# Optimization experiments

Hardware: AMD Instinct MI355X
Metric: run time of the kernel (lower is better)

## Reference

```python
import jax, jax.numpy as jnp
import numpy as np

FACTOR = 2  # self.factor
KSIZE = 3   # causal_fusion depthwise conv kernel size


def causal_fusion(x, w, b):
    # x: [BH, C, N]; depthwise causal conv over the node axis (left pad k-1)
    k = w.shape[-1]
    out = jax.lax.conv_general_dilated(
        x, w, window_strides=(1,), padding=[(k - 1, 0)],
        dimension_numbers=('NCH', 'OIH', 'NCH'),
        feature_group_count=x.shape[1])
    return out + b[None, :, None]


def setup_inputs() -> dict:
    key = jax.random.key(0)
    ks = jax.random.split(key, 4)
    B, N, L, H, E = 4, 64, 128, 8, 32
    queries = jax.random.normal(ks[0], (B, N, L, H, E), jnp.float32)
    keys = jax.random.normal(ks[1], (B, N, L, H, E), jnp.float32)
    values = jax.random.normal(ks[2], (B, N, L, H, E), jnp.float32)
    attn_mask = jnp.zeros((1,), jnp.bool_)
    C = E * L  # 4096 channels seen by causal_fusion
    w_cf = jax.random.normal(ks[3], (C, 1, KSIZE), jnp.float32) * 0.05
    b_cf = jnp.zeros((C,), jnp.float32)
    return {"queries": queries, "keys": keys, "values": values,
            "attn_mask": attn_mask, "w_cf": w_cf, "b_cf": b_cf}


def reference(queries, keys, values, attn_mask, w_cf, b_cf):
    B, N, L, H, E = queries.shape  # S == L, so no pad/slice branch taken

    # --- FFT cross-correlation: corr[b,n,h,e,:] = irfft(rfft(mean_n q) * conj(rfft(k)))
    qm = jnp.broadcast_to(jnp.mean(queries, axis=1, keepdims=True), queries.shape)
    qp = jnp.transpose(qm, (0, 1, 3, 4, 2))      # [B,N,H,E,L]
    kp = jnp.transpose(keys, (0, 1, 3, 4, 2))    # [B,N,H,E,L]
    vp = jnp.transpose(values, (0, 1, 3, 4, 2))  # [B,N,H,E,L]
    corr = jnp.fft.irfft(jnp.fft.rfft(qp, axis=-1) * jnp.conj(jnp.fft.rfft(kp, axis=-1)), n=L, axis=-1)

    # --- align_speed: top-k delays over channel-mean corr, circular roll of values
    mean_corr = jnp.mean(corr, axis=3)                      # [B,N,H,L]
    weight, delay_idx = jax.lax.top_k(mean_corr, FACTOR)    # [B,N,H,F]
    delay = L - delay_idx                                   # values in [1, L]
    ar = jnp.arange(L)
    aligned = []
    for i in range(FACTOR):
        idx = (ar[None, None, None, None, :] + delay[..., i][..., None, None]) % L  # [B,N,H,1,L]
        idx = jnp.broadcast_to(idx, vp.shape)
        aligned.append(jnp.take_along_axis(vp, idx, axis=-1))  # [B,N,H,E,L]

    BH = B * H
    delay_bh = jnp.transpose(delay, (0, 2, 1, 3)).reshape(BH, N, FACTOR)
    weight_bh = jnp.transpose(weight, (0, 2, 1, 3)).reshape(BH, N, FACTOR)

    # --- per-factor: sort nodes by delay -> causal fusion over nodes -> unsort
    causal_agg = []
    for i in range(FACTOR):
        indices = jnp.argsort(delay_bh[..., i], axis=-1)               # [BH,N]
        av = jnp.transpose(aligned[i], (0, 2, 1, 3, 4)).reshape(BH, N, E, L)
        av = av * jax.nn.sigmoid(weight_bh[..., i])[:, :, None, None]
        sorted_av = jnp.take_along_axis(av, indices[:, :, None, None], axis=1)
        x = jnp.transpose(sorted_av.reshape(BH, N, E * L), (0, 2, 1))  # [BH,E*L,N]
        x = causal_fusion(x, w_cf, b_cf)
        x = jnp.transpose(x, (0, 2, 1)).reshape(BH, N, E, L)
        rev = jnp.argsort(indices, axis=-1)
        x = jnp.take_along_axis(x, rev[:, :, None, None], axis=1)
        causal_agg.append(jnp.transpose(x.reshape(B, H, N, E, L), (0, 2, 1, 3, 4)))  # [B,N,H,E,L]

    # --- align_back_speed: inverse circular shift, mean over factors
    delay_back = L - delay  # [B,N,H,F]
    agg = jnp.zeros_like(causal_agg[0])
    for i in range(FACTOR):
        idx = (ar[None, None, None, None, :] + delay_back[..., i][..., None, None]) % L
        idx = jnp.broadcast_to(idx, causal_agg[i].shape)
        agg = agg + jnp.take_along_axis(causal_agg[i], idx, axis=-1)
    agg = agg / FACTOR

    V = jnp.transpose(agg, (0, 1, 4, 2, 3))  # [B,N,L,H,E]
    return V
```

## Files before the change

### kernel.cpp

```cpp
#include <hip/hip_runtime.h>
#include <math.h>

#define B_ 4
#define N_ 64
#define L_ 128
#define H_ 8
#define E_ 32
#define SC_ 8

typedef __attribute__((ext_vector_type(8))) short short8;
typedef __attribute__((ext_vector_type(4))) float f32x4;

__device__ __forceinline__ unsigned short f2bf(float x) {
    union { float f; unsigned u; } c; c.f = x;
    unsigned r = (c.u + 0x7fffu + ((c.u >> 16) & 1u)) >> 16;
    return (unsigned short)r;
}
__device__ __forceinline__ float bf2f(unsigned short h) {
    union { unsigned u; float f; } c; c.u = ((unsigned)h) << 16;
    return c.f;
}

__global__ __launch_bounds__(256) void k_qmean(const float* __restrict__ q,
                                               float* __restrict__ qm,
                                               const float* __restrict__ w,
                                               const float* __restrict__ bias,
                                               float* __restrict__ wT,
                                               float* __restrict__ bT,
                                               int* __restrict__ wcnt) {
    int blk = blockIdx.x;
    int b = blk >> 7, t = blk & 127;
    int tid = threadIdx.x;
    int c4 = tid & 63;
    int nq = tid >> 6;
    __shared__ double red[4][256];
    const f32x4* p = (const f32x4*)(q + (((size_t)(b * N_)) * L_ + t) * 256);
    double s0 = 0, s1 = 0, s2 = 0, s3 = 0;
    #pragma unroll 4
    for (int n = nq * 16; n < nq * 16 + 16; ++n) {
        f32x4 v = p[(size_t)n * 8192 + c4];
        s0 += (double)v.x; s1 += (double)v.y; s2 += (double)v.z; s3 += (double)v.w;
    }
    red[nq][c4 * 4 + 0] = s0;
    red[nq][c4 * 4 + 1] = s1;
    red[nq][c4 * 4 + 2] = s2;
    red[nq][c4 * 4 + 3] = s3;
    __syncthreads();
    int c = tid;
    double s = red[0][c] + red[1][c] + red[2][c] + red[3][c];
    qm[((size_t)b * 256 + c) * L_ + t] = (float)(s * (1.0 / 64.0));

    if (blk < 16) {
        int k = blk * 256 + tid;
        int e = k & 31, lp = k >> 5;
        int cc = e * L_ + lp;
        wT[k]        = w[cc * 3 + 0];
        wT[4096 + k] = w[cc * 3 + 1];
        wT[8192 + k] = w[cc * 3 + 2];
        bT[k]        = bias[cc];
    }
    if (blk == 16 && tid == 0) *wcnt = 0;
}

__global__ __launch_bounds__(512) void k_corr(const float* __restrict__ keys,
                                              const float* __restrict__ qm,
                                              float* __restrict__ part) {
    int blk = blockIdx.x;
    int sc = blk & 7; int bh = blk >> 3; int h = bh & 7; int b = bh >> 3;
    __shared__ unsigned short Ahi[4][64][40];
    __shared__ unsigned short Alo[4][64][40];
    __shared__ unsigned short Qhi[128][40];
    __shared__ unsigned short Qlo[128][40];
    int tid = threadIdx.x;
    int lane = tid & 63, w = tid >> 6;
    int mg = w & 1, ng = w >> 1;

    {
        int e = tid >> 4; int tq = (tid & 15) * 4;
        const float* qp = qm + ((size_t)b * 256 + h * 32 + e) * 128;
        #pragma unroll
        for (int hf = 0; hf < 2; ++hf) {
            int t0 = tq + hf * 64;
            float4 v = *(const float4*)(qp + t0);
            float vv[4] = {v.x, v.y, v.z, v.w};
            #pragma unroll
            for (int j = 0; j < 4; ++j) {
                unsigned short hi = f2bf(vv[j]);
                Qhi[t0 + j][e] = hi;
                Qlo[t0 + j][e] = f2bf(vv[j] - bf2f(hi));
            }
        }
    }
    int sn = tid >> 3; int se = (tid & 7) * 4;
    const float* kbase = keys + ((size_t)(b * N_ + sn) * L_) * 256 + h * 32 + se;
    #pragma unroll
    for (int p = 0; p < 2; ++p) {
        float4 v = *(const float4*)(kbase + (size_t)(sc * 16 + p) * 256);
        float vv[4] = {v.x, v.y, v.z, v.w};
        ushort4 h4, l4;
        unsigned short* hp = (unsigned short*)&h4;
        unsigned short* lp = (unsigned short*)&l4;
        #pragma unroll
        for (int j = 0; j < 4; ++j) {
            hp[j] = f2bf(vv[j]);
            lp[j] = f2bf(vv[j] - bf2f(hp[j]));
        }
        *(ushort4*)&Ahi[p][sn][se] = h4;
        *(ushort4*)&Alo[p][sn][se] = l4;
    }
    __syncthreads();

    f32x4 acc[2][2];
    #pragma unroll
    for (int i = 0; i < 2; ++i)
        #pragma unroll
        for (int j = 0; j < 2; ++j)
            acc[i][j] = (f32x4){0.f, 0.f, 0.f, 0.f};

    int eb = (lane >> 4) * 8;
    int rA0 = (mg * 2) * 16 + (lane & 15);
    int rA1 = rA0 + 16;
    int tau0 = (ng * 2) * 16 + (lane & 15);
    int tau1 = tau0 + 16;

    for (int it = 0; it < 8; ++it) {
        float4 stg0, stg1;
        if (it < 7) {
            stg0 = *(const float4*)(kbase + (size_t)(sc * 16 + 2 * it + 2) * 256);
            stg1 = *(const float4*)(kbase + (size_t)(sc * 16 + 2 * it + 3) * 256);
        }
        #pragma unroll
        for (int sp = 0; sp < 2; ++sp) {
            int p = 2 * it + sp;
            int slot = p & 3;
            int s = sc * 16 + p;
            short8 ah0 = *(const short8*)&Ahi[slot][rA0][eb];
            short8 ah1 = *(const short8*)&Ahi[slot][rA1][eb];
            short8 al0 = *(const short8*)&Alo[slot][rA0][eb];
            short8 al1 = *(const short8*)&Alo[slot][rA1][eb];
            int t0 = (s + tau0) & 127;
            int t1 = (s + tau1) & 127;
            short8 bh0 = *(const short8*)&Qhi[t0][eb];
            short8 bh1 = *(const short8*)&Qhi[t1][eb];
            short8 bl0 = *(const short8*)&Qlo[t0][eb];
            short8 bl1 = *(const short8*)&Qlo[t1][eb];
            acc[0][0] = __builtin_amdgcn_mfma_f32_16x16x32_bf16(ah0, bh0, acc[0][0], 0, 0, 0);
            acc[0][1] = __builtin_amdgcn_mfma_f32_16x16x32_bf16(ah0, bh1, acc[0][1], 0, 0, 0);
            acc[1][0] = __builtin_amdgcn_mfma_f32_16x16x32_bf16(ah1, bh0, acc[1][0], 0, 0, 0);
            acc[1][1] = __builtin_amdgcn_mfma_f32_16x16x32_bf16(ah1, bh1, acc[1][1], 0, 0, 0);
            acc[0][0] = __builtin_amdgcn_mfma_f32_16x16x32_bf16(ah0, bl0, acc[0][0], 0, 0, 0);
            acc[0][1] = __builtin_amdgcn_mfma_f32_16x16x32_bf16(ah0, bl1, acc[0][1], 0, 0, 0);
            acc[1][0] = __builtin_amdgcn_mfma_f32_16x16x32_bf16(ah1, bl0, acc[1][0], 0, 0, 0);
            acc[1][1] = __builtin_amdgcn_mfma_f32_16x16x32_bf16(ah1, bl1, acc[1][1], 0, 0, 0);
            acc[0][0] = __builtin_amdgcn_mfma_f32_16x16x32_bf16(al0, bh0, acc[0][0], 0, 0, 0);
            acc[0][1] = __builtin_amdgcn_mfma_f32_16x16x32_bf16(al0, bh1, acc[0][1], 0, 0, 0);
            acc[1][0] = __builtin_amdgcn_mfma_f32_16x16x32_bf16(al1, bh0, acc[1][0], 0, 0, 0);
            acc[1][1] = __builtin_amdgcn_mfma_f32_16x16x32_bf16(al1, bh1, acc[1][1], 0, 0, 0);
        }
        if (it < 7) {
            #pragma unroll
            for (int sp = 0; sp < 2; ++sp) {
                int p = 2 * it + 2 + sp;
                int slot = p & 3;
                float4 v = sp ? stg1 : stg0;
                float vv[4] = {v.x, v.y, v.z, v.w};
                ushort4 h4, l4;
                unsigned short* hp = (unsigned short*)&h4;
                unsigned short* lp = (unsigned short*)&l4;
                #pragma unroll
                for (int j = 0; j < 4; ++j) {
                    hp[j] = f2bf(vv[j]);
                    lp[j] = f2bf(vv[j] - bf2f(hp[j]));
                }
                *(ushort4*)&Ahi[slot][sn][se] = h4;
                *(ushort4*)&Alo[slot][sn][se] = l4;
            }
        }
        __syncthreads();
    }

    #pragma unroll
    for (int i = 0; i < 2; ++i) {
        int mt = mg * 2 + i;
        #pragma unroll
        for (int j = 0; j < 2; ++j) {
            int nt = ng * 2 + j;
            int tau = nt * 16 + (lane & 15);
            #pragma unroll
            for (int r = 0; r < 4; ++r) {
                int n = mt * 16 + (lane >> 4) * 4 + r;
                part[((((size_t)sc * B_ + b) * N_ + n) * H_ + h) * L_ + tau] = acc[i][j][r];
            }
        }
    }
}

__global__ __launch_bounds__(64) void k_topk(const float* __restrict__ part,
                                             int* __restrict__ didx,
                                             float* __restrict__ sig,
                                             int* __restrict__ flags,
                                             int* __restrict__ wlist,
                                             int* __restrict__ wcnt) {
    int blk = blockIdx.x;
    int lane = threadIdx.x;
    size_t rb = (size_t)blk * L_;
    const size_t stride = (size_t)B_ * N_ * H_ * L_;
    double s0 = 0.0, s1 = 0.0;
    for (int sc = 0; sc < SC_; ++sc) {
        s0 += (double)part[sc * stride + rb + lane];
        s1 += (double)part[sc * stride + rb + lane + 64];
    }
    float v0 = (float)(s0 * (1.0 / 32.0));
    float v1 = (float)(s1 * (1.0 / 32.0));

    float bv = v0; int bi = lane;
    if (v1 > v0) { bv = v1; bi = lane + 64; }
    #pragma unroll
    for (int m = 32; m; m >>= 1) {
        float ov = __shfl_xor(bv, m, 64);
        int   oi = __shfl_xor(bi, m, 64);
        if (ov > bv || (ov == bv && oi < bi)) { bv = ov; bi = oi; }
    }
    int i1 = bi; float w1v = bv;

    float c0 = (lane == i1) ? -INFINITY : v0;
    float c1 = (lane + 64 == i1) ? -INFINITY : v1;
    float bv2 = c0; int bi2 = lane;
    if (c1 > c0) { bv2 = c1; bi2 = lane + 64; }
    #pragma unroll
    for (int m = 32; m; m >>= 1) {
        float ov = __shfl_xor(bv2, m, 64);
        int   oi = __shfl_xor(bi2, m, 64);
        if (ov > bv2 || (ov == bv2 && oi < bi2)) { bv2 = ov; bi2 = oi; }
    }
    int i2 = bi2; float w2v = bv2;

    float d0 = (lane == i1 || lane == i2) ? -INFINITY : v0;
    float d1 = (lane + 64 == i1 || lane + 64 == i2) ? -INFINITY : v1;
    float bv3 = fmaxf(d0, d1);
    #pragma unroll
    for (int m = 32; m; m >>= 1) bv3 = fmaxf(bv3, __shfl_xor(bv3, m, 64));

    if (lane == 0) {
        didx[blk * 2 + 0] = i1;
        didx[blk * 2 + 1] = i2;
        sig[blk * 2 + 0] = 1.f / (1.f + expf(-w1v));
        sig[blk * 2 + 1] = 1.f / (1.f + expf(-w2v));
        int fl = (w2v - bv3 < 1e-3f) ? 1 : 0;
        flags[blk] = fl;
        if (fl) { int s = atomicAdd(wcnt, 1); wlist[s] = blk; }
    }
}

__global__ __launch_bounds__(256) void k_fixup(const float* __restrict__ keys,
                                               const float* __restrict__ qm,
                                               const int* __restrict__ wlist,
                                               const int* __restrict__ wcnt,
                                               double* __restrict__ vvg) {
    int cnt = *wcnt;
    __shared__ float ks_t[L_][E_];
    __shared__ float qs_t[L_][E_];
    __shared__ double red[16][17];
    int tid = threadIdx.x;
    for (int wi = blockIdx.x; wi < cnt * 8; wi += gridDim.x) {
        int row = wlist[wi >> 3]; int tg = wi & 7;
        int h = row & 7; int r = row >> 3; int n = r & 63; int b = r >> 6;
        __syncthreads();
        for (int idx = tid; idx < 1024; idx += 256) {
            int s = idx >> 3, e4 = idx & 7;
            *(float4*)&ks_t[s][e4 * 4] =
                *(const float4*)&keys[(((size_t)(b * N_ + n)) * L_ + s) * 256 + h * E_ + e4 * 4];
            int e = idx >> 5, t4 = (idx & 31) * 4;
            float4 v = *(const float4*)&qm[((size_t)b * 256 + h * E_ + e) * L_ + t4];
            float vvj[4] = {v.x, v.y, v.z, v.w};
            #pragma unroll
            for (int j = 0; j < 4; ++j) {
                int t = t4 + j;
                int col = ((((e >> 2) ^ (t & 7)) << 2) | (e & 3));
                qs_t[t][col] = vvj[j];
            }
        }
        __syncthreads();
        int tau = tg * 16 + (tid & 15);
        int g = tid >> 4;
        double a0 = 0, a1 = 0, a2 = 0, a3 = 0, a4 = 0, a5 = 0, a6 = 0, a7 = 0;
        #pragma unroll 2
        for (int s = g * 8; s < g * 8 + 8; ++s) {
            int t = (s + tau) & 127;
            int x = t & 7;
            #pragma unroll
            for (int e4 = 0; e4 < 8; e4 += 2) {
                float4 k0 = *(const float4*)&ks_t[s][e4 * 4];
                float4 k1 = *(const float4*)&ks_t[s][e4 * 4 + 4];
                float4 q0 = *(const float4*)&qs_t[t][(e4 ^ x) << 2];
                float4 q1 = *(const float4*)&qs_t[t][((e4 + 1) ^ x) << 2];
                a0 = fma((double)k0.x, (double)q0.x, a0);
                a1 = fma((double)k0.y, (double)q0.y, a1);
                a2 = fma((double)k0.z, (double)q0.z, a2);
                a3 = fma((double)k0.w, (double)q0.w, a3);
                a4 = fma((double)k1.x, (double)q1.x, a4);
                a5 = fma((double)k1.y, (double)q1.y, a5);
                a6 = fma((double)k1.z, (double)q1.z, a6);
                a7 = fma((double)k1.w, (double)q1.w, a7);
            }
        }
        red[g][tid & 15] = ((a0 + a1) + (a2 + a3)) + ((a4 + a5) + (a6 + a7));
        __syncthreads();
        if (tid < 16) {
            double s = 0;
            #pragma unroll
            for (int gg = 0; gg < 16; ++gg) s += red[gg][tid];
            vvg[(size_t)row * L_ + tg * 16 + tid] = s;
        }
    }
}

__global__ __launch_bounds__(128) void k_sort(const int* __restrict__ didx,
                                              const float* __restrict__ sig,
                                              const int* __restrict__ flags,
                                              const double* __restrict__ vvg,
                                              int4* __restrict__ gparam_i,
                                              f32x4* __restrict__ gparam_f) {
    int bh = blockIdx.x;
    int b = bh >> 3, h = bh & 7;
    int tid = threadIdx.x; int i = tid >> 6; int n = tid & 63;
    __shared__ int ds[2][64];
    __shared__ int pm[2][64];
    __shared__ int dival[2][64];
    __shared__ float sigval[2][64];
    {
        int row = (b * 64 + n) * 8 + h;
        int dv = didx[row * 2 + i];
        dival[i][n] = dv;
        sigval[i][n] = sig[row * 2 + i];
        ds[i][n] = 128 - dv;
    }
    __syncthreads();

    if (tid < 64) {
        int lane = tid;
        int myflag = flags[(b * 64 + lane) * 8 + h];
        unsigned long long msk = __ballot(myflag != 0);
        while (msk) {
            int nn = __ffsll((long long)msk) - 1; msk &= msk - 1;
            int row = (b * 64 + nn) * 8 + h;
            float v0 = (float)(vvg[(size_t)row * L_ + lane] * (1.0 / 32.0));
            float v1 = (float)(vvg[(size_t)row * L_ + lane + 64] * (1.0 / 32.0));
            float bv = v0; int bi = lane;
            if (v1 > v0) { bv = v1; bi = lane + 64; }
            #pragma unroll
            for (int m = 32; m; m >>= 1) {
                float ov = __shfl_xor(bv, m, 64);
                int   oi = __shfl_xor(bi, m, 64);
                if (ov > bv || (ov == bv && oi < bi)) { bv = ov; bi = oi; }
            }
            int i1 = bi; float w1v = bv;
            float c0 = (lane == i1) ? -INFINITY : v0;
            float c1 = (lane + 64 == i1) ? -INFINITY : v1;
            float bv2 = c0; int bi2 = lane;
            if (c1 > c0) { bv2 = c1; bi2 = lane + 64; }
            #pragma unroll
            for (int m = 32; m; m >>= 1) {
                float ov = __shfl_xor(bv2, m, 64);
                int   oi = __shfl_xor(bi2, m, 64);
                if (ov > bv2 || (ov == bv2 && oi < bi2)) { bv2 = ov; bi2 = oi; }
            }
            if (lane == 0) {
                dival[0][nn] = i1;      ds[0][nn] = 128 - i1;
                dival[1][nn] = bi2;     ds[1][nn] = 128 - bi2;
                sigval[0][nn] = 1.f / (1.f + expf(-w1v));
                sigval[1][nn] = 1.f / (1.f + expf(-bv2));
            }
        }
    }
    __syncthreads();

    int d = ds[i][n];
    int rank = 0;
    for (int m = 0; m < 64; ++m) {
        int dm = ds[i][m];
        rank += (dm < d || (dm == d && m < n)) ? 1 : 0;
    }
    pm[i][rank] = n;
    __syncthreads();
    int p1v = (rank >= 1) ? pm[i][rank - 1] : -1;
    int p2v = (rank >= 2) ? pm[i][rank - 2] : -1;

    int din = dival[i][n];
    int pq1 = (p1v >= 0) ? p1v : n;
    int pq2 = (p2v >= 0) ? p2v : n;
    int d1 = (p1v >= 0) ? ((din - dival[i][p1v]) & 127) : 0;
    int d2 = (p2v >= 0) ? ((din - dival[i][p2v]) & 127) : 0;
    float s1 = (p1v >= 0) ? sigval[i][p1v] : 0.f;
    float s2 = (p2v >= 0) ? sigval[i][p2v] : 0.f;
    int blko = (b * 64 + n) * 8 + h;
    gparam_i[blko * 2 + i] = make_int4(pq1, pq2, d1, d2);
    gparam_f[blko * 2 + i] = (f32x4){s1, s2, sigval[i][n], (float)din};
}

__global__ __launch_bounds__(256, 3) void k_out(const float* __restrict__ values,
                                                const float* __restrict__ wT,
                                                const float* __restrict__ bT,
                                                const int4* __restrict__ gparam_i,
                                                const f32x4* __restrict__ gparam_f,
                                                float* __restrict__ out) {
    int bid = blockIdx.x;
    int h = bid & 7;
    int q = (bid >> 3) & 3;
    int n = (bid >> 5) & 63;
    int b = bid >> 11;
    int blk = (b * 64 + n) * 8 + h;
    int tid = threadIdx.x; int e4 = tid & 7; int tq = tid >> 3;
    int t = q * 32 + tq;

    int4  gi0 = gparam_i[blk * 2 + 0];
    int4  gi1 = gparam_i[blk * 2 + 1];
    f32x4 gf0 = gparam_f[blk * 2 + 0];
    f32x4 gf1 = gparam_f[blk * 2 + 1];
    int di0 = (int)gf0.w, di1 = (int)gf1.w;

    const f32x4* v4 = (const f32x4*)values;
    const f32x4* w4 = (const f32x4*)wT;
    const f32x4* b4 = (const f32x4*)bT;
    f32x4* o4 = (f32x4*)out;
    const size_t base = ((size_t)b * N_) * L_ * 64 + h * 8 + e4;

    f32x4 vs  = v4[base + ((size_t)n * L_ + t) * 64];
    f32x4 va1 = v4[base + ((size_t)gi0.x * L_ + ((t + gi0.z) & 127)) * 64];
    f32x4 va2 = v4[base + ((size_t)gi0.y * L_ + ((t + gi0.w) & 127)) * 64];
    f32x4 vb1 = v4[base + ((size_t)gi1.x * L_ + ((t + gi1.z) & 127)) * 64];
    f32x4 vb2 = v4[base + ((size_t)gi1.y * L_ + ((t + gi1.w) & 127)) * 64];
    int wo0 = ((t + di0) & 127) * 8 + e4;
    int wo1 = ((t + di1) & 127) * 8 + e4;
    f32x4 bb0 = b4[wo0], w0a = w4[wo0], w1a = w4[1024 + wo0], w2a = w4[2048 + wo0];
    f32x4 bb1 = b4[wo1], w0b = w4[wo1], w1b = w4[1024 + wo1], w2b = w4[2048 + wo1];

    f32x4 acc = bb0 + bb1;
    acc += w2a * (gf0.z * vs);
    acc += w1a * (gf0.x * va1);
    acc += w0a * (gf0.y * va2);
    acc += w2b * (gf1.z * vs);
    acc += w1b * (gf1.x * vb1);
    acc += w0b * (gf1.y * vb2);
    o4[base + ((size_t)n * L_ + t) * 64] = acc * 0.5f;
}

extern "C" void kernel_launch(void* const* d_in, const int* in_sizes, int n_in,
                              void* d_out, int out_size, void* d_ws, size_t ws_size,
                              hipStream_t stream) {
    const float* queries = (const float*)d_in[0];
    const float* keys    = (const float*)d_in[1];
    const float* values  = (const float*)d_in[2];
    const float* w_cf = (const float*)d_in[4];
    const float* b_cf = (const float*)d_in[5];
    float* out = (float*)d_out;

    float* ws    = (float*)d_ws;
    float* qm    = ws;
    float* wT    = qm + 131072;
    float* bT    = wT + 12288;
    float* sigp  = bT + 4096;
    int*   didxp = (int*)(sigp + 4096);
    int*   flags = didxp + 4096;
    int*   wlist = flags + 2048;
    int*   wcnt  = wlist + 2048;
    double* vvg  = (double*)(wcnt + 4);
    int4*  gpi   = (int4*)(vvg + 2048 * 128);
    f32x4* gpf   = (f32x4*)(gpi + 4096);

    float* part = (float*)d_out;

    k_qmean <<<512,  256, 0, stream>>>(queries, qm, w_cf, b_cf, wT, bT, wcnt);
    k_corr  <<<256,  512, 0, stream>>>(keys, qm, part);
    k_topk  <<<2048, 64,  0, stream>>>(part, didxp, sigp, flags, wlist, wcnt);
    k_fixup <<<256,  256, 0, stream>>>(keys, qm, wlist, wcnt, vvg);
    k_sort  <<<32,   128, 0, stream>>>(didxp, sigp, flags, vvg, gpi, gpf);
    k_out   <<<8192, 256, 0, stream>>>(values, wT, bT, gpi, gpf, out);
}
```

Before: 71.97 us.

## Fuse top-k, double-precision fixup and sort into one per-(b,h) select kernel

Replaces the k_topk, k_fixup and k_sort kernels with a single k_select kernel: one 1024-thread block per (batch, head). It reduces the partial correlations, picks the top-2 delays, recomputes ambiguous rows in double precision, and ranks and sorts delays, all in shared memory. This removes two kernel launches, the global atomics and work list, and the global round-trips for flags, indices and fixup sums. The cost is that the stage now runs on only 32 blocks, and flagged rows are recomputed one after another inside a block instead of spread across 256 blocks.

```diff
diff --git a/kernel.cpp b/kernel.cpp
--- a/kernel.cpp
+++ b/kernel.cpp
@@ -26,8 +26,7 @@
                                                const float* __restrict__ w,
                                                const float* __restrict__ bias,
                                                float* __restrict__ wT,
-                                               float* __restrict__ bT,
-                                               int* __restrict__ wcnt) {
+                                               float* __restrict__ bT) {
     int blk = blockIdx.x;
     int b = blk >> 7, t = blk & 127;
     int tid = threadIdx.x;
@@ -59,7 +58,6 @@
         wT[8192 + k] = w[cc * 3 + 2];
         bT[k]        = bias[cc];
     }
-    if (blk == 16 && tid == 0) *wcnt = 0;
 }
 
 __global__ __launch_bounds__(512) void k_corr(const float* __restrict__ keys,
@@ -195,157 +193,122 @@
     }
 }
 
-__global__ __launch_bounds__(64) void k_topk(const float* __restrict__ part,
-                                             int* __restrict__ didx,
-                                             float* __restrict__ sig,
-                                             int* __restrict__ flags,
-                                             int* __restrict__ wlist,
-                                             int* __restrict__ wcnt) {
-    int blk = blockIdx.x;
-    int lane = threadIdx.x;
-    size_t rb = (size_t)blk * L_;
-    const size_t stride = (size_t)B_ * N_ * H_ * L_;
-    double s0 = 0.0, s1 = 0.0;
-    for (int sc = 0; sc < SC_; ++sc) {
-        s0 += (double)part[sc * stride + rb + lane];
-        s1 += (double)part[sc * stride + rb + lane + 64];
-    }
-    float v0 = (float)(s0 * (1.0 / 32.0));
-    float v1 = (float)(s1 * (1.0 / 32.0));
-
-    float bv = v0; int bi = lane;
-    if (v1 > v0) { bv = v1; bi = lane + 64; }
-    #pragma unroll
-    for (int m = 32; m; m >>= 1) {
-        float ov = __shfl_xor(bv, m, 64);
-        int   oi = __shfl_xor(bi, m, 64);
-        if (ov > bv || (ov == bv && oi < bi)) { bv = ov; bi = oi; }
-    }
-    int i1 = bi; float w1v = bv;
-
-    float c0 = (lane == i1) ? -INFINITY : v0;
-    float c1 = (lane + 64 == i1) ? -INFINITY : v1;
-    float bv2 = c0; int bi2 = lane;
-    if (c1 > c0) { bv2 = c1; bi2 = lane + 64; }
-    #pragma unroll
-    for (int m = 32; m; m >>= 1) {
-        float ov = __shfl_xor(bv2, m, 64);
-        int   oi = __shfl_xor(bi2, m, 64);
-        if (ov > bv2 || (ov == bv2 && oi < bi2)) { bv2 = ov; bi2 = oi; }
-    }
-    int i2 = bi2; float w2v = bv2;
-
-    float d0 = (lane == i1 || lane == i2) ? -INFINITY : v0;
-    float d1 = (lane + 64 == i1 || lane + 64 == i2) ? -INFINITY : v1;
-    float bv3 = fmaxf(d0, d1);
-    #pragma unroll
-    for (int m = 32; m; m >>= 1) bv3 = fmaxf(bv3, __shfl_xor(bv3, m, 64));
-
-    if (lane == 0) {
-        didx[blk * 2 + 0] = i1;
-        didx[blk * 2 + 1] = i2;
-        sig[blk * 2 + 0] = 1.f / (1.f + expf(-w1v));
-        sig[blk * 2 + 1] = 1.f / (1.f + expf(-w2v));
-        int fl = (w2v - bv3 < 1e-3f) ? 1 : 0;
-        flags[blk] = fl;
-        if (fl) { int s = atomicAdd(wcnt, 1); wlist[s] = blk; }
-    }
-}
-
-__global__ __launch_bounds__(256) void k_fixup(const float* __restrict__ keys,
-                                               const float* __restrict__ qm,
-                                               const int* __restrict__ wlist,
-                                               const int* __restrict__ wcnt,
-                                               double* __restrict__ vvg) {
-    int cnt = *wcnt;
+__global__ __launch_bounds__(1024) void k_select(const float* __restrict__ part,
+                                                 const float* __restrict__ keys,
+                                                 const float* __restrict__ qm,
+                                                 int4* __restrict__ gparam_i,
+                                                 f32x4* __restrict__ gparam_f) {
+    int bh = blockIdx.x;
+    int b = bh >> 3, h = bh & 7;
+    int tid = threadIdx.x;
+    int lane = tid & 63, w = tid >> 6;
+
     __shared__ float ks_t[L_][E_];
     __shared__ float qs_t[L_][E_];
-    __shared__ double red[16][17];
-    int tid = threadIdx.x;
-    for (int wi = blockIdx.x; wi < cnt * 8; wi += gridDim.x) {
-        int row = wlist[wi >> 3]; int tg = wi & 7;
-        int h = row & 7; int r = row >> 3; int n = r & 63; int b = r >> 6;
+    __shared__ double vv[8][L_];
+    __shared__ int   didxL[2][64];
+    __shared__ float sigL[2][64];
+    __shared__ int   flagL[64];
+    __shared__ int   ds[2][64];
+    __shared__ int   pm[2][64];
+
+    {
+        int e = tid >> 5, t4 = (tid & 31) * 4;
+        float4 v = *(const float4*)&qm[((size_t)b * 256 + h * E_ + e) * L_ + t4];
+        float vvj[4] = {v.x, v.y, v.z, v.w};
+        #pragma unroll
+        for (int j = 0; j < 4; ++j) {
+            int t = t4 + j;
+            int col = ((((e >> 2) ^ (t & 7)) << 2) | (e & 3));
+            qs_t[t][col] = vvj[j];
+        }
+    }
+
+    const size_t stride = (size_t)B_ * N_ * H_ * L_;
+    for (int k = 0; k < 4; ++k) {
+        int n = w * 4 + k;
+        size_t rb = (((size_t)b * 64 + n) * 8 + h) * (size_t)L_;
+        double s0 = 0.0, s1 = 0.0;
+        for (int sc = 0; sc < SC_; ++sc) {
+            s0 += (double)part[sc * stride + rb + lane];
+            s1 += (double)part[sc * stride + rb + lane + 64];
+        }
+        float v0 = (float)(s0 * (1.0 / 32.0));
+        float v1 = (float)(s1 * (1.0 / 32.0));
+
+        float bv = v0; int bi = lane;
+        if (v1 > v0) { bv = v1; bi = lane + 64; }
+        #pragma unroll
+        for (int m = 32; m; m >>= 1) {
+            float ov = __shfl_xor(bv, m, 64);
+            int   oi = __shfl_xor(bi, m, 64);
+            if (ov > bv || (ov == bv && oi < bi)) { bv = ov; bi = oi; }
+        }
+        int i1 = bi; float w1v = bv;
+
+        float c0 = (lane == i1) ? -INFINITY : v0;
+        float c1 = (lane + 64 == i1) ? -INFINITY : v1;
+        float bv2 = c0; int bi2 = lane;
+        if (c1 > c0) { bv2 = c1; bi2 = lane + 64; }
+        #pragma unroll
+        for (int m = 32; m; m >>= 1) {
+            float ov = __shfl_xor(bv2, m, 64);
+            int   oi = __shfl_xor(bi2, m, 64);
+            if (ov > bv2 || (ov == bv2 && oi < bi2)) { bv2 = ov; bi2 = oi; }
+        }
+        int i2 = bi2; float w2v = bv2;
+
+        float d0 = (lane == i1 || lane == i2) ? -INFINITY : v0;
+        float d1 = (lane + 64 == i1 || lane + 64 == i2) ? -INFINITY : v1;
+        float bv3 = fmaxf(d0, d1);
+        #pragma unroll
+        for (int m = 32; m; m >>= 1) bv3 = fmaxf(bv3, __shfl_xor(bv3, m, 64));
+
+        if (lane == 0) {
+            didxL[0][n] = i1; didxL[1][n] = i2;
+            sigL[0][n] = 1.f / (1.f + expf(-w1v));
+            sigL[1][n] = 1.f / (1.f + expf(-w2v));
+            flagL[n] = (w2v - bv3 < 1e-3f) ? 1 : 0;
+        }
+    }
+    __syncthreads();
+
+    for (int nn = 0; nn < 64; ++nn) {
+        if (!flagL[nn]) continue;
+        {
+            int s = tid >> 3, e4 = tid & 7;
+            *(float4*)&ks_t[s][e4 * 4] =
+                *(const float4*)&keys[(((size_t)(b * N_ + nn)) * L_ + s) * 256 + h * E_ + e4 * 4];
+        }
         __syncthreads();
-        for (int idx = tid; idx < 1024; idx += 256) {
-            int s = idx >> 3, e4 = idx & 7;
-            *(float4*)&ks_t[s][e4 * 4] =
-                *(const float4*)&keys[(((size_t)(b * N_ + n)) * L_ + s) * 256 + h * E_ + e4 * 4];
-            int e = idx >> 5, t4 = (idx & 31) * 4;
-            float4 v = *(const float4*)&qm[((size_t)b * 256 + h * E_ + e) * L_ + t4];
-            float vvj[4] = {v.x, v.y, v.z, v.w};
-            #pragma unroll
-            for (int j = 0; j < 4; ++j) {
-                int t = t4 + j;
-                int col = ((((e >> 2) ^ (t & 7)) << 2) | (e & 3));
-                qs_t[t][col] = vvj[j];
-            }
-        }
-        __syncthreads();
-        int tau = tg * 16 + (tid & 15);
-        int g = tid >> 4;
+        int tau = tid & 127, g = tid >> 7;
+        int sh = g >> 2, eo = g & 3;
         double a0 = 0, a1 = 0, a2 = 0, a3 = 0, a4 = 0, a5 = 0, a6 = 0, a7 = 0;
-        #pragma unroll 2
-        for (int s = g * 8; s < g * 8 + 8; ++s) {
+        for (int s = sh * 64; s < sh * 64 + 64; ++s) {
             int t = (s + tau) & 127;
             int x = t & 7;
-            #pragma unroll
-            for (int e4 = 0; e4 < 8; e4 += 2) {
-                float4 k0 = *(const float4*)&ks_t[s][e4 * 4];
-                float4 k1 = *(const float4*)&ks_t[s][e4 * 4 + 4];
-                float4 q0 = *(const float4*)&qs_t[t][(e4 ^ x) << 2];
-                float4 q1 = *(const float4*)&qs_t[t][((e4 + 1) ^ x) << 2];
-                a0 = fma((double)k0.x, (double)q0.x, a0);
-                a1 = fma((double)k0.y, (double)q0.y, a1);
-                a2 = fma((double)k0.z, (double)q0.z, a2);
-                a3 = fma((double)k0.w, (double)q0.w, a3);
-                a4 = fma((double)k1.x, (double)q1.x, a4);
-                a5 = fma((double)k1.y, (double)q1.y, a5);
-                a6 = fma((double)k1.z, (double)q1.z, a6);
-                a7 = fma((double)k1.w, (double)q1.w, a7);
-            }
-        }
-        red[g][tid & 15] = ((a0 + a1) + (a2 + a3)) + ((a4 + a5) + (a6 + a7));
+            float4 k0 = *(const float4*)&ks_t[s][eo * 8];
+            float4 k1 = *(const float4*)&ks_t[s][eo * 8 + 4];
+            float4 q0 = *(const float4*)&qs_t[t][((2 * eo) ^ x) << 2];
+            float4 q1 = *(const float4*)&qs_t[t][((2 * eo + 1) ^ x) << 2];
+            a0 = fma((double)k0.x, (double)q0.x, a0);
+            a1 = fma((double)k0.y, (double)q0.y, a1);
+            a2 = fma((double)k0.z, (double)q0.z, a2);
+            a3 = fma((double)k0.w, (double)q0.w, a3);
+            a4 = fma((double)k1.x, (double)q1.x, a4);
+            a5 = fma((double)k1.y, (double)q1.y, a5);
+            a6 = fma((double)k1.z, (double)q1.z, a6);
+            a7 = fma((double)k1.w, (double)q1.w, a7);
+        }
+        vv[g][tau] = ((a0 + a1) + (a2 + a3)) + ((a4 + a5) + (a6 + a7));
         __syncthreads();
-        if (tid < 16) {
-            double s = 0;
-            #pragma unroll
-            for (int gg = 0; gg < 16; ++gg) s += red[gg][tid];
-            vvg[(size_t)row * L_ + tg * 16 + tid] = s;
-        }
-    }
-}
-
-__global__ __launch_bounds__(128) void k_sort(const int* __restrict__ didx,
-                                              const float* __restrict__ sig,
-                                              const int* __restrict__ flags,
-                                              const double* __restrict__ vvg,
-                                              int4* __restrict__ gparam_i,
-                                              f32x4* __restrict__ gparam_f) {
-    int bh = blockIdx.x;
-    int b = bh >> 3, h = bh & 7;
-    int tid = threadIdx.x; int i = tid >> 6; int n = tid & 63;
-    __shared__ int ds[2][64];
-    __shared__ int pm[2][64];
-    __shared__ int dival[2][64];
-    __shared__ float sigval[2][64];
-    {
-        int row = (b * 64 + n) * 8 + h;
-        int dv = didx[row * 2 + i];
-        dival[i][n] = dv;
-        sigval[i][n] = sig[row * 2 + i];
-        ds[i][n] = 128 - dv;
-    }
-    __syncthreads();
-
-    if (tid < 64) {
-        int lane = tid;
-        int myflag = flags[(b * 64 + lane) * 8 + h];
-        unsigned long long msk = __ballot(myflag != 0);
-        while (msk) {
-            int nn = __ffsll((long long)msk) - 1; msk &= msk - 1;
-            int row = (b * 64 + nn) * 8 + h;
-            float v0 = (float)(vvg[(size_t)row * L_ + lane] * (1.0 / 32.0));
-            float v1 = (float)(vvg[(size_t)row * L_ + lane + 64] * (1.0 / 32.0));
+        if (tid < 64) {
+            double t0 = 0, t1 = 0;
+            #pragma unroll
+            for (int g2 = 0; g2 < 8; ++g2) { t0 += vv[g2][lane]; t1 += vv[g2][lane + 64]; }
+            float v0 = (float)(t0 * (1.0 / 32.0));
+            float v1 = (float)(t1 * (1.0 / 32.0));
+
             float bv = v0; int bi = lane;
             if (v1 > v0) { bv = v1; bi = lane + 64; }
             #pragma unroll
@@ -355,6 +318,7 @@
                 if (ov > bv || (ov == bv && oi < bi)) { bv = ov; bi = oi; }
             }
             int i1 = bi; float w1v = bv;
+
             float c0 = (lane == i1) ? -INFINITY : v0;
             float c1 = (lane + 64 == i1) ? -INFINITY : v1;
             float bv2 = c0; int bi2 = lane;
@@ -366,36 +330,41 @@
                 if (ov > bv2 || (ov == bv2 && oi < bi2)) { bv2 = ov; bi2 = oi; }
             }
             if (lane == 0) {
-                dival[0][nn] = i1;      ds[0][nn] = 128 - i1;
-                dival[1][nn] = bi2;     ds[1][nn] = 128 - bi2;
-                sigval[0][nn] = 1.f / (1.f + expf(-w1v));
-                sigval[1][nn] = 1.f / (1.f + expf(-bv2));
-            }
-        }
-    }
+                didxL[0][nn] = i1; didxL[1][nn] = bi2;
+                sigL[0][nn] = 1.f / (1.f + expf(-w1v));
+                sigL[1][nn] = 1.f / (1.f + expf(-bv2));
+            }
+        }
+        __syncthreads();
+    }
+
+    int ii = tid >> 6, n2 = tid & 63;
+    int rank = 0;
+    if (tid < 128) ds[ii][n2] = 128 - didxL[ii][n2];
     __syncthreads();
-
-    int d = ds[i][n];
-    int rank = 0;
-    for (int m = 0; m < 64; ++m) {
-        int dm = ds[i][m];
-        rank += (dm < d || (dm == d && m < n)) ? 1 : 0;
-    }
-    pm[i][rank] = n;
+    if (tid < 128) {
+        int d = ds[ii][n2];
+        for (int m = 0; m < 64; ++m) {
+            int dm = ds[ii][m];
+            rank += (dm < d || (dm == d && m < n2)) ? 1 : 0;
+        }
+        pm[ii][rank] = n2;
+    }
     __syncthreads();
-    int p1v = (rank >= 1) ? pm[i][rank - 1] : -1;
-    int p2v = (rank >= 2) ? pm[i][rank - 2] : -1;
-
-    int din = dival[i][n];
-    int pq1 = (p1v >= 0) ? p1v : n;
-    int pq2 = (p2v >= 0) ? p2v : n;
-    int d1 = (p1v >= 0) ? ((din - dival[i][p1v]) & 127) : 0;
-    int d2 = (p2v >= 0) ? ((din - dival[i][p2v]) & 127) : 0;
-    float s1 = (p1v >= 0) ? sigval[i][p1v] : 0.f;
-    float s2 = (p2v >= 0) ? sigval[i][p2v] : 0.f;
-    int blko = (b * 64 + n) * 8 + h;
-    gparam_i[blko * 2 + i] = make_int4(pq1, pq2, d1, d2);
-    gparam_f[blko * 2 + i] = (f32x4){s1, s2, sigval[i][n], (float)din};
+    if (tid < 128) {
+        int p1v = (rank >= 1) ? pm[ii][rank - 1] : -1;
+        int p2v = (rank >= 2) ? pm[ii][rank - 2] : -1;
+        int din = didxL[ii][n2];
+        int pq1 = (p1v >= 0) ? p1v : n2;
+        int pq2 = (p2v >= 0) ? p2v : n2;
+        int d1 = (p1v >= 0) ? ((din - didxL[ii][p1v]) & 127) : 0;
+        int d2 = (p2v >= 0) ? ((din - didxL[ii][p2v]) & 127) : 0;
+        float s1 = (p1v >= 0) ? sigL[ii][p1v] : 0.f;
+        float s2 = (p2v >= 0) ? sigL[ii][p2v] : 0.f;
+        int blko = (b * 64 + n2) * 8 + h;
+        gparam_i[blko * 2 + ii] = make_int4(pq1, pq2, d1, d2);
+        gparam_f[blko * 2 + ii] = (f32x4){s1, s2, sigL[ii][n2], (float)din};
+    }
 }
 
 __global__ __launch_bounds__(256, 3) void k_out(const float* __restrict__ values,
@@ -459,21 +428,13 @@
     float* qm    = ws;
     float* wT    = qm + 131072;
     float* bT    = wT + 12288;
-    float* sigp  = bT + 4096;
-    int*   didxp = (int*)(sigp + 4096);
-    int*   flags = didxp + 4096;
-    int*   wlist = flags + 2048;
-    int*   wcnt  = wlist + 2048;
-    double* vvg  = (double*)(wcnt + 4);
-    int4*  gpi   = (int4*)(vvg + 2048 * 128);
+    int4*  gpi   = (int4*)(bT + 4096);
     f32x4* gpf   = (f32x4*)(gpi + 4096);
 
     float* part = (float*)d_out;
 
-    k_qmean <<<512,  256, 0, stream>>>(queries, qm, w_cf, b_cf, wT, bT, wcnt);
-    k_corr  <<<256,  512, 0, stream>>>(keys, qm, part);
-    k_topk  <<<2048, 64,  0, stream>>>(part, didxp, sigp, flags, wlist, wcnt);
-    k_fixup <<<256,  256, 0, stream>>>(keys, qm, wlist, wcnt, vvg);
-    k_sort  <<<32,   128, 0, stream>>>(didxp, sigp, flags, vvg, gpi, gpf);
-    k_out   <<<8192, 256, 0, stream>>>(values, wT, bT, gpi, gpf, out);
-}
+    k_qmean  <<<512,  256,  0, stream>>>(queries, qm, w_cf, b_cf, wT, bT);
+    k_corr   <<<256,  512,  0, stream>>>(keys, qm, part);
+    k_select <<<32,   1024, 0, stream>>>(part, keys, qm, gpi, gpf);
+    k_out    <<<8192, 256,  0, stream>>>(values, wT, bT, gpi, gpf, out);
+}
```

New measurement: 137.4 us. 90.9% more time.
